# Kernel tuning notes

Hardware: AMD Instinct MI355X
Metric: run time of the kernel (lower is better)

## Reference

```python
import jax, jax.numpy as jnp
import numpy as np

N = 524288   # sparse points
C = 64       # io channels
AC = 128     # attn channels
H = 8        # heads
PS = 64      # patch size
HID = 256    # mlp hidden (mlp_ratio=2)
HD = AC // H # head dim
EPS = 1e-5


def _ln(x):
    mu = x.mean(-1, keepdims=True)
    v = x.var(-1, keepdims=True)
    return (x - mu) / jnp.sqrt(v + EPS)


def setup_inputs() -> dict:
    key = jax.random.key(0)
    ks = jax.random.split(key, 12)
    def w(k, shape, fan_in):
        return jax.random.normal(k, shape, jnp.float32) * (1.0 / np.sqrt(fan_in))
    return {
        "feats": jax.random.normal(ks[0], (N, C), jnp.float32),
        "w_pre": w(ks[1], (C, AC), C),    "b_pre": jnp.zeros((AC,), jnp.float32),
        "g1": jnp.ones((AC,), jnp.float32), "b1": jnp.zeros((AC,), jnp.float32),
        "w_qkv": w(ks[2], (AC, 3 * AC), AC), "b_qkv": jnp.zeros((3 * AC,), jnp.float32),
        "w_proj": w(ks[3], (AC, AC), AC), "b_proj": jnp.zeros((AC,), jnp.float32),
        "g2": jnp.ones((AC,), jnp.float32), "b2": jnp.zeros((AC,), jnp.float32),
        "w_m1": w(ks[4], (AC, HID), AC),  "b_m1": jnp.zeros((HID,), jnp.float32),
        "w_m2": w(ks[5], (HID, AC), HID), "b_m2": jnp.zeros((AC,), jnp.float32),
        "w_post": w(ks[6], (AC, C), AC),  "b_post": jnp.zeros((C,), jnp.float32),
    }


def reference(feats, w_pre, b_pre, g1, b1, w_qkv, b_qkv, w_proj, b_proj,
              g2, b2, w_m1, b_m1, w_m2, b_m2, w_post, b_post):
    # pre_proj: 1x1 sparse conv == pointwise linear on [N, C]
    x2 = feats @ w_pre + b_pre                            # [N, AC]
    # norm1 -> patch attention
    n1 = _ln(x2) * g1 + b1
    P = N // PS
    qkv = (n1 @ w_qkv + b_qkv).reshape(P, PS, 3, H, HD)   # patches of 64 pts
    q, k, v = qkv[:, :, 0], qkv[:, :, 1], qkv[:, :, 2]    # [P, PS, H, HD]
    scale = HD ** -0.5
    att = jnp.einsum('pqhd,pkhd->phqk', q, k) * scale     # [P, H, PS, PS]
    att = jax.nn.softmax(att, axis=-1)
    o = jnp.einsum('phqk,pkhd->pqhd', att, v).reshape(N, AC)
    h = o @ w_proj + b_proj
    x2 = x2 + h                                           # residual 1
    # norm2 -> pointwise MLP (1x1 conv -> GELU -> 1x1 conv)
    n2 = _ln(x2) * g2 + b2
    h2 = jax.nn.gelu(n2 @ w_m1 + b_m1, approximate=False) @ w_m2 + b_m2
    x2 = x2 + h2                                          # residual 2
    return x2 @ w_post + b_post                           # post_proj [N, C]
```

## Files before the change

### kernel.cpp

```cpp
#include <hip/hip_runtime.h>
#include <hip/hip_bf16.h>
#include <math.h>


typedef __bf16 bf16;
typedef __bf16 bf16x8 __attribute__((ext_vector_type(8)));
typedef __bf16 bf16x4 __attribute__((ext_vector_type(4)));
typedef float  f32x4  __attribute__((ext_vector_type(4)));

#define MFMA16(a, b, c) __builtin_amdgcn_mfma_f32_16x16x32_bf16((a), (b), (c), 0, 0, 0)

constexpr int OFF_PRE  = 0;
constexpr int OFF_QKV  = 8192;
constexpr int OFF_PROJ = 57344;
constexpr int OFF_M1   = 73728;
constexpr int OFF_M2   = 106496;
constexpr int OFF_POST = 139264;

template <int W>
__device__ __forceinline__ int swz(int row, int col) {
    constexpr int CH = W >> 3;
    constexpr int M  = (CH - 1) < 15 ? (CH - 1) : 15;
    const int c = (col >> 3) ^ (row & M);
    return row * W + c * 8 + (col & 7);
}

__device__ __forceinline__ bf16x8 zero8() {
    bf16x8 z;
#pragma unroll
    for (int j = 0; j < 8; ++j) z[j] = (bf16)0.0f;
    return z;
}

__device__ __forceinline__ void st4(bf16* p, const f32x4 v) {
    bf16x4 o;
#pragma unroll
    for (int r = 0; r < 4; ++r) o[r] = (bf16)v[r];
    *(bf16x4*)p = o;
}

__device__ __forceinline__ float gelu_f(float x) {
    const float u = 0.79788456f * x * (1.0f + 0.044715f * x * x);
    const float e = __builtin_amdgcn_exp2f(u * 2.8853900817779268f);
    return x - x * __builtin_amdgcn_rcpf(e + 1.0f);
}

__global__ void pack_all(const float* __restrict__ w_pre,
                         const float* __restrict__ w_qkv,
                         const float* __restrict__ w_proj,
                         const float* __restrict__ w_m1,
                         const float* __restrict__ w_m2,
                         const float* __restrict__ w_post,
                         bf16* __restrict__ dst) {
    const int t = blockIdx.x;
    const float* src;
    int Ncol, KT, off, t0;
    if (t < 16)       { src = w_pre;  Ncol = 128; KT = 2; off = OFF_PRE;  t0 = 0; }
    else if (t < 112) { src = w_qkv;  Ncol = 384; KT = 4; off = OFF_QKV;  t0 = 16; }
    else if (t < 144) { src = w_proj; Ncol = 128; KT = 4; off = OFF_PROJ; t0 = 112; }
    else if (t < 208) { src = w_m1;   Ncol = 256; KT = 4; off = OFF_M1;   t0 = 144; }
    else if (t < 272) { src = w_m2;   Ncol = 128; KT = 8; off = OFF_M2;   t0 = 208; }
    else              { src = w_post; Ncol = 64;  KT = 4; off = OFF_POST; t0 = 272; }
    const int tile = t - t0;
    const int lane = threadIdx.x;
    const int mt = tile / KT, kt = tile - mt * KT;
    const int n  = mt * 16 + (lane & 15);
    const int k0 = kt * 32 + (lane >> 4) * 8;
    bf16x8 v;
#pragma unroll
    for (int j = 0; j < 8; ++j) v[j] = (bf16)src[(k0 + j) * Ncol + n];
    *(bf16x8*)(dst + off + ((long)(tile * 64 + lane)) * 8) = v;
}

__device__ __forceinline__ void ln_rows(const bf16* __restrict__ in,
                                        bf16* __restrict__ outb,
                                        const float* __restrict__ g,
                                        const float* __restrict__ b, int tid) {
    const int row = tid >> 3, sub = tid & 7;
    bf16x8 c0 = *(const bf16x8*)(in + swz<128>(row, sub * 16));
    bf16x8 c1 = *(const bf16x8*)(in + swz<128>(row, sub * 16 + 8));
    float v[16];
#pragma unroll
    for (int j = 0; j < 8; ++j) { v[j] = (float)c0[j]; v[8 + j] = (float)c1[j]; }
    float s = 0.f, ss = 0.f;
#pragma unroll
    for (int j = 0; j < 16; ++j) { s += v[j]; ss += v[j] * v[j]; }
#pragma unroll
    for (int m = 1; m <= 4; m <<= 1) {
        s += __shfl_xor(s, m);
        ss += __shfl_xor(ss, m);
    }
    const float mu   = s * (1.0f / 128.0f);
    const float rstd = __builtin_amdgcn_rsqf(ss * (1.0f / 128.0f) - mu * mu + 1e-5f);
    bf16x8 o0, o1;
#pragma unroll
    for (int j = 0; j < 8; ++j) {
        o0[j] = (bf16)((v[j] - mu) * rstd * g[sub * 16 + j] + b[sub * 16 + j]);
        o1[j] = (bf16)((v[8 + j] - mu) * rstd * g[sub * 16 + 8 + j] + b[sub * 16 + 8 + j]);
    }
    *(bf16x8*)(outb + swz<128>(row, sub * 16)) = o0;
    *(bf16x8*)(outb + swz<128>(row, sub * 16 + 8)) = o1;
}

__global__ __launch_bounds__(512, 4)
void fused_block_kernel(const float* __restrict__ feats,
                        const bf16* __restrict__ wp,
                        const float* __restrict__ b_pre,
                        const float* __restrict__ g1, const float* __restrict__ b1,
                        const float* __restrict__ b_qkv,
                        const float* __restrict__ b_proj,
                        const float* __restrict__ g2, const float* __restrict__ b2,
                        const float* __restrict__ b_m1,
                        const float* __restrict__ b_m2,
                        const float* __restrict__ b_post,
                        float* __restrict__ out) {
    __shared__ __align__(16) bf16 R1[64 * 128];
    __shared__ __align__(16) bf16 R2[64 * 128];
    __shared__ __align__(16) bf16 R34[64 * 256];
    bf16* const R3 = R34;
    bf16* const R4 = R34 + 64 * 128;

    const int tid  = threadIdx.x;
    const int w    = tid >> 6;
    const int lane = tid & 63;
    const int q    = lane >> 4;
    const int l15  = lane & 15;
    const long base = (long)blockIdx.x * 64;
    const f32x4 fzero = {0.f, 0.f, 0.f, 0.f};

    {
        const int row = tid >> 3, ch = tid & 7;
        const float* src = feats + (base + row) * 64 + ch * 8;
        float4 a = *(const float4*)src;
        float4 b = *(const float4*)(src + 4);
        bf16x8 v;
        v[0] = (bf16)a.x; v[1] = (bf16)a.y; v[2] = (bf16)a.z; v[3] = (bf16)a.w;
        v[4] = (bf16)b.x; v[5] = (bf16)b.y; v[6] = (bf16)b.z; v[7] = (bf16)b.w;
        *(bf16x8*)(R2 + swz<64>(row, ch * 8)) = v;
    }
    __syncthreads();

    f32x4 x2[4];

    {
        f32x4 acc[4];
#pragma unroll
        for (int tt = 0; tt < 4; ++tt) acc[tt] = fzero;
#pragma unroll
        for (int ks = 0; ks < 2; ++ks) {
            bf16x8 afr = *(const bf16x8*)(wp + OFF_PRE + ((w * 2 + ks) * 64 + lane) * 8);
#pragma unroll
            for (int tt = 0; tt < 4; ++tt) {
                bf16x8 bfr = *(const bf16x8*)(R2 + swz<64>(tt * 16 + l15, ks * 32 + q * 8));
                acc[tt] = MFMA16(afr, bfr, acc[tt]);
            }
        }
        const f32x4 bias = *(const f32x4*)(b_pre + w * 16 + q * 4);
#pragma unroll
        for (int tt = 0; tt < 4; ++tt) {
#pragma unroll
            for (int r = 0; r < 4; ++r) x2[tt][r] = acc[tt][r] + bias[r];
            st4(R3 + swz<128>(tt * 16 + l15, w * 16 + q * 4), x2[tt]);
        }
    }
    __syncthreads();

    ln_rows(R3, R1, g1, b1, tid);
    __syncthreads();

    {
        bf16x8 B[4][4];
#pragma unroll
        for (int ks = 0; ks < 4; ++ks)
#pragma unroll
            for (int tt = 0; tt < 4; ++tt)
                B[ks][tt] = *(const bf16x8*)(R1 + swz<128>(tt * 16 + l15, ks * 32 + q * 8));
#pragma unroll
        for (int part = 0; part < 3; ++part) {
            const int mt = part * 8 + w;
            f32x4 acc[4];
#pragma unroll
            for (int tt = 0; tt < 4; ++tt) acc[tt] = fzero;
#pragma unroll
            for (int ks = 0; ks < 4; ++ks) {
                bf16x8 afr = *(const bf16x8*)(wp + OFF_QKV + ((mt * 4 + ks) * 64 + lane) * 8);
#pragma unroll
                for (int tt = 0; tt < 4; ++tt) acc[tt] = MFMA16(afr, B[ks][tt], acc[tt]);
            }
            const f32x4 bias = *(const f32x4*)(b_qkv + mt * 16 + q * 4);
            if (part == 0) {
#pragma unroll
                for (int tt = 0; tt < 4; ++tt)
                    st4(R2 + swz<128>(tt * 16 + l15, w * 16 + q * 4), acc[tt] + bias);
            } else if (part == 1) {
#pragma unroll
                for (int tt = 0; tt < 4; ++tt)
                    st4(R3 + swz<128>(tt * 16 + l15, w * 16 + q * 4), acc[tt] + bias);
            } else {
#pragma unroll
                for (int tt = 0; tt < 4; ++tt)
#pragma unroll
                    for (int r = 0; r < 4; ++r)
                        R4[w * 1024 + swz<64>(q * 4 + r, tt * 16 + l15)] =
                            (bf16)(acc[tt][r] + bias[r]);
            }
        }
    }
    __syncthreads();

    {
        const int colA = w * 16 + (q & 1) * 8;
        const bool hi = (q >= 2);
        const bf16x8 z8 = zero8();
        bf16x8 Kf[4];
#pragma unroll
        for (int kt = 0; kt < 4; ++kt) {
            bf16x8 t = *(const bf16x8*)(R3 + swz<128>(kt * 16 + l15, colA));
            Kf[kt] = hi ? z8 : t;
        }
#pragma unroll
        for (int qt = 0; qt < 4; ++qt) {
            bf16x8 t = *(const bf16x8*)(R2 + swz<128>(qt * 16 + l15, colA));
            bf16x8 Qf = hi ? z8 : t;
            f32x4 S[4];
#pragma unroll
            for (int kt = 0; kt < 4; ++kt) S[kt] = MFMA16(Kf[kt], Qf, fzero);
            float P[4][4];
            float mx = -1e30f;
#pragma unroll
            for (int kt = 0; kt < 4; ++kt)
#pragma unroll
                for (int r = 0; r < 4; ++r) {
                    const float sv = S[kt][r] * 0.25f;
                    P[kt][r] = sv;
                    mx = fmaxf(mx, sv);
                }
            mx = fmaxf(mx, __shfl_xor(mx, 16));
            mx = fmaxf(mx, __shfl_xor(mx, 32));
            float lsum = 0.f;
#pragma unroll
            for (int kt = 0; kt < 4; ++kt)
#pragma unroll
                for (int r = 0; r < 4; ++r) {
                    const float e = __builtin_amdgcn_exp2f((P[kt][r] - mx) * 1.4426950408889634f);
                    P[kt][r] = e;
                    lsum += e;
                }
            lsum += __shfl_xor(lsum, 16);
            lsum += __shfl_xor(lsum, 32);
            const float inv = __builtin_amdgcn_rcpf(lsum);
#pragma unroll
            for (int kt = 0; kt < 4; ++kt)
#pragma unroll
                for (int r = 0; r < 4; ++r) P[kt][r] *= inv;
            f32x4 O = fzero;
#pragma unroll
            for (int ks = 0; ks < 2; ++ks) {
                bf16x8 Bf;
#pragma unroll
                for (int j = 0; j < 8; ++j) {
                    const int src = (((q & 1) * 2 + (j >> 2)) << 4) + l15;
                    const float v0 = __shfl(P[ks * 2][j & 3], src);
                    const float v1 = __shfl(P[ks * 2 + 1][j & 3], src);
                    Bf[j] = (bf16)((q >> 1) ? v1 : v0);
                }
                bf16x8 Af = *(const bf16x8*)(R4 + w * 1024 + swz<64>(l15, ks * 32 + q * 8));
                O = MFMA16(Af, Bf, O);
            }
            st4(R1 + swz<128>(qt * 16 + l15, w * 16 + q * 4), O);
        }
    }
    __syncthreads();

    {
        f32x4 acc[4];
#pragma unroll
        for (int tt = 0; tt < 4; ++tt) acc[tt] = fzero;
#pragma unroll
        for (int ks = 0; ks < 4; ++ks) {
            bf16x8 afr = *(const bf16x8*)(wp + OFF_PROJ + ((w * 4 + ks) * 64 + lane) * 8);
#pragma unroll
            for (int tt = 0; tt < 4; ++tt) {
                bf16x8 bfr = *(const bf16x8*)(R1 + swz<128>(tt * 16 + l15, ks * 32 + q * 8));
                acc[tt] = MFMA16(afr, bfr, acc[tt]);
            }
        }
        const f32x4 bias = *(const f32x4*)(b_proj + w * 16 + q * 4);
#pragma unroll
        for (int tt = 0; tt < 4; ++tt) {
#pragma unroll
            for (int r = 0; r < 4; ++r) x2[tt][r] += acc[tt][r] + bias[r];
            st4(R3 + swz<128>(tt * 16 + l15, w * 16 + q * 4), x2[tt]);
        }
    }
    __syncthreads();

    ln_rows(R3, R1, g2, b2, tid);
    __syncthreads();

    {
        bf16x8 B[4][4];
#pragma unroll
        for (int ks = 0; ks < 4; ++ks)
#pragma unroll
            for (int tt = 0; tt < 4; ++tt)
                B[ks][tt] = *(const bf16x8*)(R1 + swz<128>(tt * 16 + l15, ks * 32 + q * 8));
#pragma unroll
        for (int half = 0; half < 2; ++half) {
            const int mt = w * 2 + half;
            f32x4 acc[4];
#pragma unroll
            for (int tt = 0; tt < 4; ++tt) acc[tt] = fzero;
#pragma unroll
            for (int ks = 0; ks < 4; ++ks) {
                bf16x8 afr = *(const bf16x8*)(wp + OFF_M1 + ((mt * 4 + ks) * 64 + lane) * 8);
#pragma unroll
                for (int tt = 0; tt < 4; ++tt) acc[tt] = MFMA16(afr, B[ks][tt], acc[tt]);
            }
            const f32x4 bias = *(const f32x4*)(b_m1 + mt * 16 + q * 4);
#pragma unroll
            for (int tt = 0; tt < 4; ++tt) {
                f32x4 gl;
#pragma unroll
                for (int r = 0; r < 4; ++r) gl[r] = gelu_f(acc[tt][r] + bias[r]);
                st4(R34 + swz<256>(tt * 16 + l15, mt * 16 + q * 4), gl);
            }
        }
    }
    __syncthreads();

    {
        f32x4 acc[4];
#pragma unroll
        for (int tt = 0; tt < 4; ++tt) acc[tt] = fzero;
#pragma unroll
        for (int ks = 0; ks < 8; ++ks) {
            bf16x8 afr = *(const bf16x8*)(wp + OFF_M2 + ((w * 8 + ks) * 64 + lane) * 8);
#pragma unroll
            for (int tt = 0; tt < 4; ++tt) {
                bf16x8 bfr = *(const bf16x8*)(R34 + swz<256>(tt * 16 + l15, ks * 32 + q * 8));
                acc[tt] = MFMA16(afr, bfr, acc[tt]);
            }
        }
        const f32x4 bias = *(const f32x4*)(b_m2 + w * 16 + q * 4);
#pragma unroll
        for (int tt = 0; tt < 4; ++tt) {
#pragma unroll
            for (int r = 0; r < 4; ++r) x2[tt][r] += acc[tt][r] + bias[r];
            st4(R1 + swz<128>(tt * 16 + l15, w * 16 + q * 4), x2[tt]);
        }
    }
    __syncthreads();

    {
        const int ct  = w >> 1;
        const int tt0 = (w & 1) * 2;
        f32x4 acc[2];
#pragma unroll
        for (int rr = 0; rr < 2; ++rr) acc[rr] = fzero;
#pragma unroll
        for (int ks = 0; ks < 4; ++ks) {
            bf16x8 afr = *(const bf16x8*)(wp + OFF_POST + ((ct * 4 + ks) * 64 + lane) * 8);
#pragma unroll
            for (int rr = 0; rr < 2; ++rr) {
                bf16x8 bfr = *(const bf16x8*)(R1 + swz<128>((tt0 + rr) * 16 + l15, ks * 32 + q * 8));
                acc[rr] = MFMA16(afr, bfr, acc[rr]);
            }
        }
        const f32x4 bias = *(const f32x4*)(b_post + ct * 16 + q * 4);
#pragma unroll
        for (int rr = 0; rr < 2; ++rr) {
            f32x4 v = acc[rr] + bias;
            *(f32x4*)(out + (base + (tt0 + rr) * 16 + l15) * 64 + ct * 16 + q * 4) = v;
        }
    }
}

extern "C" void kernel_launch(void* const* d_in, const int* in_sizes, int n_in,
                              void* d_out, int out_size, void* d_ws, size_t ws_size,
                              hipStream_t stream) {
    const float* feats  = (const float*)d_in[0];
    const float* w_pre  = (const float*)d_in[1];
    const float* b_pre  = (const float*)d_in[2];
    const float* g1     = (const float*)d_in[3];
    const float* b1     = (const float*)d_in[4];
    const float* w_qkv  = (const float*)d_in[5];
    const float* b_qkv  = (const float*)d_in[6];
    const float* w_proj = (const float*)d_in[7];
    const float* b_proj = (const float*)d_in[8];
    const float* g2     = (const float*)d_in[9];
    const float* b2     = (const float*)d_in[10];
    const float* w_m1   = (const float*)d_in[11];
    const float* b_m1   = (const float*)d_in[12];
    const float* w_m2   = (const float*)d_in[13];
    const float* b_m2   = (const float*)d_in[14];
    const float* w_post = (const float*)d_in[15];
    const float* b_post = (const float*)d_in[16];

    bf16* wp = (bf16*)d_ws;

    pack_all<<<288, 64, 0, stream>>>(w_pre, w_qkv, w_proj, w_m1, w_m2, w_post, wp);

    fused_block_kernel<<<8192, 512, 0, stream>>>(
        feats, wp, b_pre, g1, b1, b_qkv, b_proj, g2, b2, b_m1, b_m2, b_post,
        (float*)d_out);
}
```

Before: 636.7 us.

## Shrink LDS footprint to three buffers and raise occupancy to six blocks

Cuts shared memory from 64KB to 48KB per block by keeping Q in registers, which are redistributed with shuffles instead of staged through LDS, and by splitting the MLP hidden activations across two 128-wide buffers. The launch bound asks for 6 blocks of 512 threads per CU instead of 4, to raise wave occupancy and hide latency. To fit the register budget, the cached B-fragment arrays for the QKV and MLP1 GEMMs are dropped and reloaded from LDS inside the loops. The risks are more LDS reads and shuffle work, plus possible spills under the tighter register limit.

```diff
diff --git a/kernel.cpp b/kernel.cpp
--- a/kernel.cpp
+++ b/kernel.cpp
@@ -102,7 +102,7 @@
     *(bf16x8*)(outb + swz<128>(row, sub * 16 + 8)) = o1;
 }
 
-__global__ __launch_bounds__(512, 4)
+__global__ __launch_bounds__(512, 6)
 void fused_block_kernel(const float* __restrict__ feats,
                         const bf16* __restrict__ wp,
                         const float* __restrict__ b_pre,
@@ -114,11 +114,9 @@
                         const float* __restrict__ b_m2,
                         const float* __restrict__ b_post,
                         float* __restrict__ out) {
-    __shared__ __align__(16) bf16 R1[64 * 128];
-    __shared__ __align__(16) bf16 R2[64 * 128];
-    __shared__ __align__(16) bf16 R34[64 * 256];
-    bf16* const R3 = R34;
-    bf16* const R4 = R34 + 64 * 128;
+    __shared__ __align__(16) bf16 Ra[64 * 128];
+    __shared__ __align__(16) bf16 Rb[64 * 128];
+    __shared__ __align__(16) bf16 Rc[64 * 128];
 
     const int tid  = threadIdx.x;
     const int w    = tid >> 6;
@@ -136,11 +134,12 @@
         bf16x8 v;
         v[0] = (bf16)a.x; v[1] = (bf16)a.y; v[2] = (bf16)a.z; v[3] = (bf16)a.w;
         v[4] = (bf16)b.x; v[5] = (bf16)b.y; v[6] = (bf16)b.z; v[7] = (bf16)b.w;
-        *(bf16x8*)(R2 + swz<64>(row, ch * 8)) = v;
+        *(bf16x8*)(Ra + swz<64>(row, ch * 8)) = v;
     }
     __syncthreads();
 
     f32x4 x2[4];
+    f32x4 Qacc[4];
 
     {
         f32x4 acc[4];
@@ -151,7 +150,7 @@
             bf16x8 afr = *(const bf16x8*)(wp + OFF_PRE + ((w * 2 + ks) * 64 + lane) * 8);
 #pragma unroll
             for (int tt = 0; tt < 4; ++tt) {
-                bf16x8 bfr = *(const bf16x8*)(R2 + swz<64>(tt * 16 + l15, ks * 32 + q * 8));
+                bf16x8 bfr = *(const bf16x8*)(Ra + swz<64>(tt * 16 + l15, ks * 32 + q * 8));
                 acc[tt] = MFMA16(afr, bfr, acc[tt]);
             }
         }
@@ -160,21 +159,15 @@
         for (int tt = 0; tt < 4; ++tt) {
 #pragma unroll
             for (int r = 0; r < 4; ++r) x2[tt][r] = acc[tt][r] + bias[r];
-            st4(R3 + swz<128>(tt * 16 + l15, w * 16 + q * 4), x2[tt]);
-        }
-    }
-    __syncthreads();
-
-    ln_rows(R3, R1, g1, b1, tid);
-    __syncthreads();
-
-    {
-        bf16x8 B[4][4];
-#pragma unroll
-        for (int ks = 0; ks < 4; ++ks)
-#pragma unroll
-            for (int tt = 0; tt < 4; ++tt)
-                B[ks][tt] = *(const bf16x8*)(R1 + swz<128>(tt * 16 + l15, ks * 32 + q * 8));
+            st4(Rb + swz<128>(tt * 16 + l15, w * 16 + q * 4), x2[tt]);
+        }
+    }
+    __syncthreads();
+
+    ln_rows(Rb, Rc, g1, b1, tid);
+    __syncthreads();
+
+    {
 #pragma unroll
         for (int part = 0; part < 3; ++part) {
             const int mt = part * 8 + w;
@@ -185,23 +178,25 @@
             for (int ks = 0; ks < 4; ++ks) {
                 bf16x8 afr = *(const bf16x8*)(wp + OFF_QKV + ((mt * 4 + ks) * 64 + lane) * 8);
 #pragma unroll
-                for (int tt = 0; tt < 4; ++tt) acc[tt] = MFMA16(afr, B[ks][tt], acc[tt]);
+                for (int tt = 0; tt < 4; ++tt) {
+                    bf16x8 bfr = *(const bf16x8*)(Rc + swz<128>(tt * 16 + l15, ks * 32 + q * 8));
+                    acc[tt] = MFMA16(afr, bfr, acc[tt]);
+                }
             }
             const f32x4 bias = *(const f32x4*)(b_qkv + mt * 16 + q * 4);
             if (part == 0) {
 #pragma unroll
+                for (int tt = 0; tt < 4; ++tt) Qacc[tt] = acc[tt] + bias;
+            } else if (part == 1) {
+#pragma unroll
                 for (int tt = 0; tt < 4; ++tt)
-                    st4(R2 + swz<128>(tt * 16 + l15, w * 16 + q * 4), acc[tt] + bias);
-            } else if (part == 1) {
+                    st4(Rb + swz<128>(tt * 16 + l15, w * 16 + q * 4), acc[tt] + bias);
+            } else {
 #pragma unroll
                 for (int tt = 0; tt < 4; ++tt)
-                    st4(R3 + swz<128>(tt * 16 + l15, w * 16 + q * 4), acc[tt] + bias);
-            } else {
-#pragma unroll
-                for (int tt = 0; tt < 4; ++tt)
 #pragma unroll
                     for (int r = 0; r < 4; ++r)
-                        R4[w * 1024 + swz<64>(q * 4 + r, tt * 16 + l15)] =
+                        Ra[w * 1024 + swz<64>(q * 4 + r, tt * 16 + l15)] =
                             (bf16)(acc[tt][r] + bias[r]);
             }
         }
@@ -215,13 +210,18 @@
         bf16x8 Kf[4];
 #pragma unroll
         for (int kt = 0; kt < 4; ++kt) {
-            bf16x8 t = *(const bf16x8*)(R3 + swz<128>(kt * 16 + l15, colA));
+            bf16x8 t = *(const bf16x8*)(Rb + swz<128>(kt * 16 + l15, colA));
             Kf[kt] = hi ? z8 : t;
         }
 #pragma unroll
         for (int qt = 0; qt < 4; ++qt) {
-            bf16x8 t = *(const bf16x8*)(R2 + swz<128>(qt * 16 + l15, colA));
-            bf16x8 Qf = hi ? z8 : t;
+            bf16x8 Qf;
+#pragma unroll
+            for (int j = 0; j < 8; ++j) {
+                const int src = (((q & 1) * 2 + (j >> 2)) << 4) + l15;
+                const float v = __shfl(Qacc[qt][j & 3], src);
+                Qf[j] = hi ? (bf16)0.0f : (bf16)v;
+            }
             f32x4 S[4];
 #pragma unroll
             for (int kt = 0; kt < 4; ++kt) S[kt] = MFMA16(Kf[kt], Qf, fzero);
@@ -264,10 +264,10 @@
                     const float v1 = __shfl(P[ks * 2 + 1][j & 3], src);
                     Bf[j] = (bf16)((q >> 1) ? v1 : v0);
                 }
-                bf16x8 Af = *(const bf16x8*)(R4 + w * 1024 + swz<64>(l15, ks * 32 + q * 8));
+                bf16x8 Af = *(const bf16x8*)(Ra + w * 1024 + swz<64>(l15, ks * 32 + q * 8));
                 O = MFMA16(Af, Bf, O);
             }
-            st4(R1 + swz<128>(qt * 16 + l15, w * 16 + q * 4), O);
+            st4(Rc + swz<128>(qt * 16 + l15, w * 16 + q * 4), O);
         }
     }
     __syncthreads();
@@ -281,7 +281,7 @@
             bf16x8 afr = *(const bf16x8*)(wp + OFF_PROJ + ((w * 4 + ks) * 64 + lane) * 8);
 #pragma unroll
             for (int tt = 0; tt < 4; ++tt) {
-                bf16x8 bfr = *(const bf16x8*)(R1 + swz<128>(tt * 16 + l15, ks * 32 + q * 8));
+                bf16x8 bfr = *(const bf16x8*)(Rc + swz<128>(tt * 16 + l15, ks * 32 + q * 8));
                 acc[tt] = MFMA16(afr, bfr, acc[tt]);
             }
         }
@@ -290,24 +290,19 @@
         for (int tt = 0; tt < 4; ++tt) {
 #pragma unroll
             for (int r = 0; r < 4; ++r) x2[tt][r] += acc[tt][r] + bias[r];
-            st4(R3 + swz<128>(tt * 16 + l15, w * 16 + q * 4), x2[tt]);
-        }
-    }
-    __syncthreads();
-
-    ln_rows(R3, R1, g2, b2, tid);
-    __syncthreads();
-
-    {
-        bf16x8 B[4][4];
-#pragma unroll
-        for (int ks = 0; ks < 4; ++ks)
-#pragma unroll
-            for (int tt = 0; tt < 4; ++tt)
-                B[ks][tt] = *(const bf16x8*)(R1 + swz<128>(tt * 16 + l15, ks * 32 + q * 8));
-#pragma unroll
-        for (int half = 0; half < 2; ++half) {
-            const int mt = w * 2 + half;
+            st4(Rb + swz<128>(tt * 16 + l15, w * 16 + q * 4), x2[tt]);
+        }
+    }
+    __syncthreads();
+
+    ln_rows(Rb, Rc, g2, b2, tid);
+    __syncthreads();
+
+    {
+#pragma unroll
+        for (int h = 0; h < 2; ++h) {
+            const int mt = h * 8 + w;
+            bf16* const dst = h ? Rb : Ra;
             f32x4 acc[4];
 #pragma unroll
             for (int tt = 0; tt < 4; ++tt) acc[tt] = fzero;
@@ -315,7 +310,10 @@
             for (int ks = 0; ks < 4; ++ks) {
                 bf16x8 afr = *(const bf16x8*)(wp + OFF_M1 + ((mt * 4 + ks) * 64 + lane) * 8);
 #pragma unroll
-                for (int tt = 0; tt < 4; ++tt) acc[tt] = MFMA16(afr, B[ks][tt], acc[tt]);
+                for (int tt = 0; tt < 4; ++tt) {
+                    bf16x8 bfr = *(const bf16x8*)(Rc + swz<128>(tt * 16 + l15, ks * 32 + q * 8));
+                    acc[tt] = MFMA16(afr, bfr, acc[tt]);
+                }
             }
             const f32x4 bias = *(const f32x4*)(b_m1 + mt * 16 + q * 4);
 #pragma unroll
@@ -323,7 +321,7 @@
                 f32x4 gl;
 #pragma unroll
                 for (int r = 0; r < 4; ++r) gl[r] = gelu_f(acc[tt][r] + bias[r]);
-                st4(R34 + swz<256>(tt * 16 + l15, mt * 16 + q * 4), gl);
+                st4(dst + swz<128>(tt * 16 + l15, w * 16 + q * 4), gl);
             }
         }
     }
@@ -335,10 +333,12 @@
         for (int tt = 0; tt < 4; ++tt) acc[tt] = fzero;
 #pragma unroll
         for (int ks = 0; ks < 8; ++ks) {
+            const bf16* const srcR = (ks < 4) ? Ra : Rb;
+            const int col = (ks & 3) * 32 + q * 8;
             bf16x8 afr = *(const bf16x8*)(wp + OFF_M2 + ((w * 8 + ks) * 64 + lane) * 8);
 #pragma unroll
             for (int tt = 0; tt < 4; ++tt) {
-                bf16x8 bfr = *(const bf16x8*)(R34 + swz<256>(tt * 16 + l15, ks * 32 + q * 8));
+                bf16x8 bfr = *(const bf16x8*)(srcR + swz<128>(tt * 16 + l15, col));
                 acc[tt] = MFMA16(afr, bfr, acc[tt]);
             }
         }
@@ -347,7 +347,7 @@
         for (int tt = 0; tt < 4; ++tt) {
 #pragma unroll
             for (int r = 0; r < 4; ++r) x2[tt][r] += acc[tt][r] + bias[r];
-            st4(R1 + swz<128>(tt * 16 + l15, w * 16 + q * 4), x2[tt]);
+            st4(Rc + swz<128>(tt * 16 + l15, w * 16 + q * 4), x2[tt]);
         }
     }
     __syncthreads();
@@ -363,7 +363,7 @@
             bf16x8 afr = *(const bf16x8*)(wp + OFF_POST + ((ct * 4 + ks) * 64 + lane) * 8);
 #pragma unroll
             for (int rr = 0; rr < 2; ++rr) {
-                bf16x8 bfr = *(const bf16x8*)(R1 + swz<128>((tt0 + rr) * 16 + l15, ks * 32 + q * 8));
+                bf16x8 bfr = *(const bf16x8*)(Rc + swz<128>((tt0 + rr) * 16 + l15, ks * 32 + q * 8));
                 acc[rr] = MFMA16(afr, bfr, acc[rr]);
             }
         }
```

Measured after the change: 698.5 us. 1.1x slower.
